# Kernel optimization log

Hardware: AMD Instinct MI355X
Metric: run time of the kernel (lower is better)

## Reference

```python
import jax, jax.numpy as jnp
import numpy as np

B, S, F_IN, F_OUT, K = 4, 4096, 64, 64, 32


def setup_inputs() -> dict:
    key = jax.random.key(0)
    k1, k2, k3 = jax.random.split(key, 3)
    X = jax.random.normal(k1, (B, S, F_IN), dtype=jnp.float32)
    M = jax.random.normal(k2, (B, S, K), dtype=jnp.float32)
    # xavier_uniform for weight: bound = sqrt(6/(fan_in+fan_out))
    bound = float(np.sqrt(6.0 / (F_IN + F_OUT)))
    weight = jax.random.uniform(k3, (F_IN, F_OUT), dtype=jnp.float32,
                                minval=-bound, maxval=bound)
    bias = jnp.zeros((F_OUT,), dtype=jnp.float32)
    return {"X": X, "M": M, "weight": weight, "bias": bias}


def reference(X, M, weight, bias):
    # similarity = softmax(relu(M M^T), axis=-1)  -> [B, S, S]
    sim_raw = jnp.einsum('bsk,btk->bst', M, M)
    sim = jax.nn.softmax(jax.nn.relu(sim_raw), axis=-1)
    # X W  -> [B, S, F_OUT]
    Xw = jnp.einsum('bsf,fo->bso', X, weight)
    # mode='add': (I + A) Xw = Xw + A @ Xw  (identity matmul folded)
    Z = Xw + jnp.einsum('bst,bto->bso', sim, Xw)
    Z = Z + bias
    # dropout is identity at inference (eval mode)
    return Z
```

## Files before the change

kernel.cpp:

```cpp
#include <hip/hip_runtime.h>
#include <cstdint>

#define BATCH  4
#define SLEN   4096
#define FDIM   64
#define KDIM   32
#define KSPLIT 8
#define CHUNK  (SLEN / KSPLIT)

typedef __attribute__((ext_vector_type(8))) short bf16x8;
typedef __attribute__((ext_vector_type(4))) float f32x4;

static __device__ __forceinline__ short f2bf(float f) {
    union { float f; unsigned u; } v; v.f = f;
    unsigned r = v.u + 0x7fffu + ((v.u >> 16) & 1u);
    return (short)(r >> 16);
}
static __device__ __forceinline__ float bf2f(short s) {
    union { unsigned u; float f; } v;
    v.u = ((unsigned)(unsigned short)s) << 16;
    return v.f;
}
static __device__ __forceinline__ unsigned pack2bf(float a, float b) {
    union { float f; unsigned u; } x, y; x.f = a; y.f = b;
    unsigned ra = x.u + 0x7fffu + ((x.u >> 16) & 1u);
    unsigned rb = y.u + 0x7fffu + ((y.u >> 16) & 1u);
    return __builtin_amdgcn_perm(rb, ra, 0x07060302u);
}

__global__ __launch_bounds__(256) void prep(const float4* __restrict__ M4,
                                            ushort4* __restrict__ H4,
                                            ushort4* __restrict__ L4,
                                            ushort4* __restrict__ QH4,
                                            ushort4* __restrict__ QL4,
                                            const float* __restrict__ X,
                                            const float4* __restrict__ W4,
                                            float4* __restrict__ V4,
                                            short* __restrict__ Vt) {
    const int blk = blockIdx.y * gridDim.x + blockIdx.x;
    const float LOG2E = 1.4426950408889634f;
#pragma unroll
    for (int r = 0; r < 2; ++r) {
        int i = (blk * 2 + r) * 256 + threadIdx.x;
        float4 m = M4[i];
        ushort4 h, l, sh, sl;
        h.x = (unsigned short)f2bf(m.x); l.x = (unsigned short)f2bf(m.x - bf2f((short)h.x));
        h.y = (unsigned short)f2bf(m.y); l.y = (unsigned short)f2bf(m.y - bf2f((short)h.y));
        h.z = (unsigned short)f2bf(m.z); l.z = (unsigned short)f2bf(m.z - bf2f((short)h.z));
        h.w = (unsigned short)f2bf(m.w); l.w = (unsigned short)f2bf(m.w - bf2f((short)h.w));
        float sx = m.x * LOG2E, sy = m.y * LOG2E, sz = m.z * LOG2E, sw = m.w * LOG2E;
        sh.x = (unsigned short)f2bf(sx); sl.x = (unsigned short)f2bf(sx - bf2f((short)sh.x));
        sh.y = (unsigned short)f2bf(sy); sl.y = (unsigned short)f2bf(sy - bf2f((short)sh.y));
        sh.z = (unsigned short)f2bf(sz); sl.z = (unsigned short)f2bf(sz - bf2f((short)sh.z));
        sh.w = (unsigned short)f2bf(sw); sl.w = (unsigned short)f2bf(sw - bf2f((short)sh.w));
        H4[i] = h; L4[i] = l; QH4[i] = sh; QL4[i] = sl;
    }
    __shared__ float t[64][65];
    const int b  = blockIdx.y;
    const int s0 = blockIdx.x * 64;
    const int o4 = threadIdx.x & 15;
    const int rq = threadIdx.x >> 4;
#pragma unroll
    for (int half = 0; half < 4; ++half) {
        int r = half * 16 + rq;
        const float* __restrict__ xr = X + ((size_t)b * SLEN + s0 + r) * FDIM;
        float4 acc = make_float4(0.f, 0.f, 0.f, 0.f);
#pragma unroll
        for (int f = 0; f < FDIM; ++f) {
            float4 w = W4[f * 16 + o4];
            float  x = xr[f];
            acc.x = fmaf(x, w.x, acc.x);
            acc.y = fmaf(x, w.y, acc.y);
            acc.z = fmaf(x, w.z, acc.z);
            acc.w = fmaf(x, w.w, acc.w);
        }
        V4[((size_t)b * SLEN + s0 + r) * 16 + o4] = acc;
        t[r][o4 * 4 + 0] = acc.x;
        t[r][o4 * 4 + 1] = acc.y;
        t[r][o4 * 4 + 2] = acc.z;
        t[r][o4 * 4 + 3] = acc.w;
    }
    __syncthreads();
    const int c0 = threadIdx.x & 63;
    const int r0 = threadIdx.x >> 6;
    const int pc = (c0 & 32) | (((c0 >> 2) & 3) << 3) | (((c0 >> 4) & 1) << 2)
                 | (c0 & 3);
#pragma unroll
    for (int i = 0; i < 16; ++i) {
        int f = r0 + i * 4;
        Vt[((size_t)b * FDIM + f) * SLEN + s0 + pc] = f2bf(t[c0][f]);
    }
}

__global__ __launch_bounds__(256, 4) void attn_mfma(const short* __restrict__ Mhi,
                                                    const short* __restrict__ Mlo,
                                                    const short* __restrict__ Qhi,
                                                    const short* __restrict__ Qlo,
                                                    const short* __restrict__ Vt,
                                                    float* __restrict__ accP,
                                                    float* __restrict__ lP) {
    const int bid  = blockIdx.x;
    const int slab = (bid & 7) + 8 * (bid >> 8);
    const int qblk = (bid >> 3) & 31;
    const int b    = slab >> 3;
    const int ks   = slab & 7;

    const int tid  = threadIdx.x;
    const int wave = tid >> 6;
    const int lane = tid & 63;
    const int col  = lane & 15;
    const int quad = lane >> 4;
    const int qbase = qblk * 128 + wave * 32;
    const int k0    = ks * CHUNK;

    const short* __restrict__ Mbh = Mhi + (size_t)b * SLEN * KDIM;
    const short* __restrict__ Mbl = Mlo + (size_t)b * SLEN * KDIM;
    const short* __restrict__ Qbh = Qhi + (size_t)b * SLEN * KDIM;
    const short* __restrict__ Qbl = Qlo + (size_t)b * SLEN * KDIM;
    const short* __restrict__ Vb  = Vt  + (size_t)b * FDIM * SLEN;

    __shared__ short khi[32 * 40];
    __shared__ short klo[32 * 40];
    __shared__ short vsh[64 * 40];

    bf16x8 Qh[2], Ql[2];
#pragma unroll
    for (int tq = 0; tq < 2; ++tq) {
        int qo = (qbase + tq * 16 + col) * KDIM + quad * 8;
        Qh[tq] = *(const bf16x8*)(Qbh + qo);
        Ql[tq] = *(const bf16x8*)(Qbl + qo);
    }

    const bf16x8 ONES = (bf16x8){0x3F80, 0x3F80, 0x3F80, 0x3F80,
                                 0x3F80, 0x3F80, 0x3F80, 0x3F80};

    f32x4 accf[2][4], accl[2];
#pragma unroll
    for (int tq = 0; tq < 2; ++tq) {
        accl[tq] = (f32x4){0.f, 0.f, 0.f, 0.f};
#pragma unroll
        for (int fg = 0; fg < 4; ++fg) accf[tq][fg] = (f32x4){0.f, 0.f, 0.f, 0.f};
    }

    const int krow  = (tid & 127) >> 2;
    const int kpart = tid & 3;
    const int vrow  = tid >> 2;
    const short* __restrict__ Msrc = (tid < 128) ? Mbh : Mbl;
    short* __restrict__ kdst = (tid < 128) ? khi : klo;

#pragma unroll 1
    for (int kt = k0; kt < k0 + CHUNK; kt += 32) {
        bf16x8 kstg = *(const bf16x8*)(Msrc + (kt + krow) * KDIM + kpart * 8);
        bf16x8 vstg = *(const bf16x8*)(Vb + (size_t)vrow * SLEN + kt + kpart * 8);
        __syncthreads();
        *(bf16x8*)(kdst + krow * 40 + kpart * 8) = kstg;
        *(bf16x8*)(vsh + vrow * 40 + kpart * 8)  = vstg;
        __syncthreads();

        bf16x8 Kh0 = *(const bf16x8*)(khi + col * 40 + quad * 8);
        bf16x8 Kh1 = *(const bf16x8*)(khi + (16 + col) * 40 + quad * 8);
        bf16x8 Kl0 = *(const bf16x8*)(klo + col * 40 + quad * 8);
        bf16x8 Kl1 = *(const bf16x8*)(klo + (16 + col) * 40 + quad * 8);
        bf16x8 Vv[4];
#pragma unroll
        for (int fg = 0; fg < 4; ++fg)
            Vv[fg] = *(const bf16x8*)(vsh + (fg * 16 + col) * 40 + quad * 8);

#pragma unroll
        for (int tq = 0; tq < 2; ++tq) {
            f32x4 z = (f32x4){0.f, 0.f, 0.f, 0.f};
            f32x4 c0 = __builtin_amdgcn_mfma_f32_16x16x32_bf16(Kh0, Ql[tq], z, 0, 0, 0);
            f32x4 c1 = __builtin_amdgcn_mfma_f32_16x16x32_bf16(Kh1, Ql[tq], z, 0, 0, 0);
            c0 = __builtin_amdgcn_mfma_f32_16x16x32_bf16(Kl0, Qh[tq], c0, 0, 0, 0);
            c1 = __builtin_amdgcn_mfma_f32_16x16x32_bf16(Kl1, Qh[tq], c1, 0, 0, 0);
            c0 = __builtin_amdgcn_mfma_f32_16x16x32_bf16(Kh0, Qh[tq], c0, 0, 0, 0);
            c1 = __builtin_amdgcn_mfma_f32_16x16x32_bf16(Kh1, Qh[tq], c1, 0, 0, 0);

            float e0 = __builtin_amdgcn_exp2f(fmaxf(c0[0], 0.f));
            float e1 = __builtin_amdgcn_exp2f(fmaxf(c0[1], 0.f));
            float e2 = __builtin_amdgcn_exp2f(fmaxf(c0[2], 0.f));
            float e3 = __builtin_amdgcn_exp2f(fmaxf(c0[3], 0.f));
            float e4 = __builtin_amdgcn_exp2f(fmaxf(c1[0], 0.f));
            float e5 = __builtin_amdgcn_exp2f(fmaxf(c1[1], 0.f));
            float e6 = __builtin_amdgcn_exp2f(fmaxf(c1[2], 0.f));
            float e7 = __builtin_amdgcn_exp2f(fmaxf(c1[3], 0.f));

            union { unsigned u[4]; bf16x8 v; } pa;
            pa.u[0] = pack2bf(e0, e1);
            pa.u[1] = pack2bf(e2, e3);
            pa.u[2] = pack2bf(e4, e5);
            pa.u[3] = pack2bf(e6, e7);

            accl[tq] = __builtin_amdgcn_mfma_f32_16x16x32_bf16(pa.v, ONES,
                                                               accl[tq], 0, 0, 0);
#pragma unroll
            for (int fg = 0; fg < 4; ++fg)
                accf[tq][fg] = __builtin_amdgcn_mfma_f32_16x16x32_bf16(
                    pa.v, Vv[fg], accf[tq][fg], 0, 0, 0);
        }
    }

#pragma unroll
    for (int tq = 0; tq < 2; ++tq) {
#pragma unroll
        for (int j = 0; j < 4; ++j) {
            int q = qbase + tq * 16 + quad * 4 + j;
            size_t base = ((size_t)b * SLEN + q) * KSPLIT + ks;
            float* __restrict__ op = accP + base * FDIM;
#pragma unroll
            for (int fg = 0; fg < 4; ++fg)
                op[fg * 16 + col] = accf[tq][fg][j];
            if (col == 0) lP[base] = accl[tq][j];
        }
    }
}

__global__ __launch_bounds__(256) void combine_kernel(const float4* __restrict__ V4,
                                                      const float4* __restrict__ accP4,
                                                      const float* __restrict__ lP,
                                                      const float4* __restrict__ bias4,
                                                      float4* __restrict__ out4) {
    int i  = blockIdx.x * 256 + threadIdx.x;
    int o4 = i & 15;
    int row = i >> 4;
    float nx = 0.f, ny = 0.f, nz = 0.f, nw = 0.f, den = 0.f;
#pragma unroll
    for (int k = 0; k < KSPLIT; ++k) {
        float4 a = accP4[((size_t)row * KSPLIT + k) * 16 + o4];
        nx += a.x; ny += a.y; nz += a.z; nw += a.w;
        den += lP[(size_t)row * KSPLIT + k];
    }
    float r = 1.f / den;
    float4 v = V4[i];
    float4 bb = bias4[o4];
    float4 o;
    o.x = v.x + nx * r + bb.x;
    o.y = v.y + ny * r + bb.y;
    o.z = v.z + nz * r + bb.z;
    o.w = v.w + nw * r + bb.w;
    out4[i] = o;
}

extern "C" void kernel_launch(void* const* d_in, const int* in_sizes, int n_in,
                              void* d_out, int out_size, void* d_ws, size_t ws_size,
                              hipStream_t stream) {
    const float* X    = (const float*)d_in[0];
    const float* M    = (const float*)d_in[1];
    const float* W    = (const float*)d_in[2];
    const float* bias = (const float*)d_in[3];
    float* out = (float*)d_out;

    const size_t vElems = (size_t)BATCH * SLEN * FDIM;
    const size_t mElems = (size_t)BATCH * SLEN * KDIM;
    const size_t rows   = (size_t)BATCH * SLEN;

    float* Vf   = (float*)d_ws;
    float* accP = Vf + vElems;
    float* lP   = accP + vElems * KSPLIT;
    short* Mhi  = (short*)(lP + rows * KSPLIT);
    short* Mlo  = Mhi + mElems;
    short* Qhi  = Mlo + mElems;
    short* Qlo  = Qhi + mElems;
    short* Vt   = Qlo + mElems;

    prep<<<dim3(SLEN / 64, BATCH), 256, 0, stream>>>(
        (const float4*)M, (ushort4*)Mhi, (ushort4*)Mlo,
        (ushort4*)Qhi, (ushort4*)Qlo,
        X, (const float4*)W, (float4*)Vf, Vt);

    attn_mfma<<<dim3((SLEN / 128) * BATCH * KSPLIT), 256, 0, stream>>>(
        Mhi, Mlo, Qhi, Qlo, Vt, accP, lP);

    combine_kernel<<<(int)(vElems / 1024), 256, 0, stream>>>(
        (const float4*)Vf, (const float4*)accP, lP, (const float4*)bias,
        (float4*)out);
}
```

Baseline: 122.5 us.

## Fuse split-K combine into attention kernel and load K/V directly from global

Folds the combine kernel into the attention kernel: each split-K block atomically bumps a per-query-block counter, and the last arriving block reduces the partial sums and writes the output. The LDS staging of K and V tiles and its barriers are removed, so each wave reads K and V fragments directly from global memory. The query tile per block doubles to 256 rows (64 per wave), halving the block count and lowering the occupancy hint to 2. This cuts a launch and the barriers but raises register pressure, adds redundant global loads per wave, and concentrates the reduction tail in a few blocks.

New measurement: 221.2 us. 80.5% more time.

```diff
diff --git a/kernel.cpp b/kernel.cpp
--- a/kernel.cpp
+++ b/kernel.cpp
@@ -7,6 +7,8 @@
 #define KDIM   32
 #define KSPLIT 8
 #define CHUNK  (SLEN / KSPLIT)
+#define QBLK   256
+#define NQB    (SLEN / QBLK)
 
 typedef __attribute__((ext_vector_type(8))) short bf16x8;
 typedef __attribute__((ext_vector_type(4))) float f32x4;
@@ -36,7 +38,11 @@
                                             const float* __restrict__ X,
                                             const float4* __restrict__ W4,
                                             float4* __restrict__ V4,
-                                            short* __restrict__ Vt) {
+                                            short* __restrict__ Vt,
+                                            int* __restrict__ cnt) {
+    if (blockIdx.y == 0 && threadIdx.x == 0)
+        cnt[blockIdx.x] = 0;
+
     const int blk = blockIdx.y * gridDim.x + blockIdx.x;
     const float LOG2E = 1.4426950408889634f;
 #pragma unroll
@@ -92,25 +98,31 @@
     }
 }
 
-__global__ __launch_bounds__(256, 4) void attn_mfma(const short* __restrict__ Mhi,
+__global__ __launch_bounds__(256, 2) void attn_mfma(const short* __restrict__ Mhi,
                                                     const short* __restrict__ Mlo,
                                                     const short* __restrict__ Qhi,
                                                     const short* __restrict__ Qlo,
                                                     const short* __restrict__ Vt,
                                                     float* __restrict__ accP,
-                                                    float* __restrict__ lP) {
+                                                    float* __restrict__ lP,
+                                                    const float4* __restrict__ V4,
+                                                    const float4* __restrict__ bias4,
+                                                    float4* __restrict__ out4,
+                                                    int* __restrict__ cnt) {
     const int bid  = blockIdx.x;
-    const int slab = (bid & 7) + 8 * (bid >> 8);
-    const int qblk = (bid >> 3) & 31;
-    const int b    = slab >> 3;
-    const int ks   = slab & 7;
+    const int xcd  = bid & 7;
+    const int slot = bid >> 3;
+    const int g    = xcd + 8 * (slot >> 4);
+    const int qblk = slot & 15;
+    const int b    = g >> 3;
+    const int ks   = g & 7;
 
     const int tid  = threadIdx.x;
     const int wave = tid >> 6;
     const int lane = tid & 63;
     const int col  = lane & 15;
     const int quad = lane >> 4;
-    const int qbase = qblk * 128 + wave * 32;
+    const int qbase = qblk * QBLK + wave * 64;
     const int k0    = ks * CHUNK;
 
     const short* __restrict__ Mbh = Mhi + (size_t)b * SLEN * KDIM;
@@ -119,13 +131,9 @@
     const short* __restrict__ Qbl = Qlo + (size_t)b * SLEN * KDIM;
     const short* __restrict__ Vb  = Vt  + (size_t)b * FDIM * SLEN;
 
-    __shared__ short khi[32 * 40];
-    __shared__ short klo[32 * 40];
-    __shared__ short vsh[64 * 40];
-
-    bf16x8 Qh[2], Ql[2];
-#pragma unroll
-    for (int tq = 0; tq < 2; ++tq) {
+    bf16x8 Qh[4], Ql[4];
+#pragma unroll
+    for (int tq = 0; tq < 4; ++tq) {
         int qo = (qbase + tq * 16 + col) * KDIM + quad * 8;
         Qh[tq] = *(const bf16x8*)(Qbh + qo);
         Ql[tq] = *(const bf16x8*)(Qbl + qo);
@@ -134,40 +142,27 @@
     const bf16x8 ONES = (bf16x8){0x3F80, 0x3F80, 0x3F80, 0x3F80,
                                  0x3F80, 0x3F80, 0x3F80, 0x3F80};
 
-    f32x4 accf[2][4], accl[2];
-#pragma unroll
-    for (int tq = 0; tq < 2; ++tq) {
+    f32x4 accf[4][4], accl[4];
+#pragma unroll
+    for (int tq = 0; tq < 4; ++tq) {
         accl[tq] = (f32x4){0.f, 0.f, 0.f, 0.f};
 #pragma unroll
         for (int fg = 0; fg < 4; ++fg) accf[tq][fg] = (f32x4){0.f, 0.f, 0.f, 0.f};
     }
-
-    const int krow  = (tid & 127) >> 2;
-    const int kpart = tid & 3;
-    const int vrow  = tid >> 2;
-    const short* __restrict__ Msrc = (tid < 128) ? Mbh : Mbl;
-    short* __restrict__ kdst = (tid < 128) ? khi : klo;
 
 #pragma unroll 1
     for (int kt = k0; kt < k0 + CHUNK; kt += 32) {
-        bf16x8 kstg = *(const bf16x8*)(Msrc + (kt + krow) * KDIM + kpart * 8);
-        bf16x8 vstg = *(const bf16x8*)(Vb + (size_t)vrow * SLEN + kt + kpart * 8);
-        __syncthreads();
-        *(bf16x8*)(kdst + krow * 40 + kpart * 8) = kstg;
-        *(bf16x8*)(vsh + vrow * 40 + kpart * 8)  = vstg;
-        __syncthreads();
-
-        bf16x8 Kh0 = *(const bf16x8*)(khi + col * 40 + quad * 8);
-        bf16x8 Kh1 = *(const bf16x8*)(khi + (16 + col) * 40 + quad * 8);
-        bf16x8 Kl0 = *(const bf16x8*)(klo + col * 40 + quad * 8);
-        bf16x8 Kl1 = *(const bf16x8*)(klo + (16 + col) * 40 + quad * 8);
+        const bf16x8 Kh0 = *(const bf16x8*)(Mbh + (kt + col) * KDIM + quad * 8);
+        const bf16x8 Kh1 = *(const bf16x8*)(Mbh + (kt + 16 + col) * KDIM + quad * 8);
+        const bf16x8 Kl0 = *(const bf16x8*)(Mbl + (kt + col) * KDIM + quad * 8);
+        const bf16x8 Kl1 = *(const bf16x8*)(Mbl + (kt + 16 + col) * KDIM + quad * 8);
         bf16x8 Vv[4];
 #pragma unroll
         for (int fg = 0; fg < 4; ++fg)
-            Vv[fg] = *(const bf16x8*)(vsh + (fg * 16 + col) * 40 + quad * 8);
-
-#pragma unroll
-        for (int tq = 0; tq < 2; ++tq) {
+            Vv[fg] = *(const bf16x8*)(Vb + (fg * 16 + col) * SLEN + kt + quad * 8);
+
+#pragma unroll
+        for (int tq = 0; tq < 4; ++tq) {
             f32x4 z = (f32x4){0.f, 0.f, 0.f, 0.f};
             f32x4 c0 = __builtin_amdgcn_mfma_f32_16x16x32_bf16(Kh0, Ql[tq], z, 0, 0, 0);
             f32x4 c1 = __builtin_amdgcn_mfma_f32_16x16x32_bf16(Kh1, Ql[tq], z, 0, 0, 0);
@@ -201,7 +196,7 @@
     }
 
 #pragma unroll
-    for (int tq = 0; tq < 2; ++tq) {
+    for (int tq = 0; tq < 4; ++tq) {
 #pragma unroll
         for (int j = 0; j < 4; ++j) {
             int q = qbase + tq * 16 + quad * 4 + j;
@@ -213,32 +208,41 @@
             if (col == 0) lP[base] = accl[tq][j];
         }
     }
-}
-
-__global__ __launch_bounds__(256) void combine_kernel(const float4* __restrict__ V4,
-                                                      const float4* __restrict__ accP4,
-                                                      const float* __restrict__ lP,
-                                                      const float4* __restrict__ bias4,
-                                                      float4* __restrict__ out4) {
-    int i  = blockIdx.x * 256 + threadIdx.x;
-    int o4 = i & 15;
-    int row = i >> 4;
-    float nx = 0.f, ny = 0.f, nz = 0.f, nw = 0.f, den = 0.f;
-#pragma unroll
-    for (int k = 0; k < KSPLIT; ++k) {
-        float4 a = accP4[((size_t)row * KSPLIT + k) * 16 + o4];
-        nx += a.x; ny += a.y; nz += a.z; nw += a.w;
-        den += lP[(size_t)row * KSPLIT + k];
-    }
-    float r = 1.f / den;
-    float4 v = V4[i];
-    float4 bb = bias4[o4];
-    float4 o;
-    o.x = v.x + nx * r + bb.x;
-    o.y = v.y + ny * r + bb.y;
-    o.z = v.z + nz * r + bb.z;
-    o.w = v.w + nw * r + bb.w;
-    out4[i] = o;
+
+    __threadfence();
+    __syncthreads();
+    __shared__ int lastFlag;
+    if (tid == 0) {
+        int old = atomicAdd(&cnt[b * NQB + qblk], 1);
+        lastFlag = (old == KSPLIT - 1) ? 1 : 0;
+    }
+    __syncthreads();
+    if (lastFlag) {
+        __threadfence();
+        const int o4   = tid & 15;
+        const int rsub = tid >> 4;
+        const float4 bb = bias4[o4];
+        const float4* __restrict__ accP4 = (const float4*)accP;
+#pragma unroll 1
+        for (int it = 0; it < 16; ++it) {
+            size_t row = (size_t)b * SLEN + qblk * QBLK + it * 16 + rsub;
+            float nx = 0.f, ny = 0.f, nz = 0.f, nw = 0.f, den = 0.f;
+#pragma unroll
+            for (int k = 0; k < KSPLIT; ++k) {
+                float4 a = accP4[(row * KSPLIT + k) * 16 + o4];
+                nx += a.x; ny += a.y; nz += a.z; nw += a.w;
+                den += lP[row * KSPLIT + k];
+            }
+            float rr = 1.f / den;
+            float4 v = V4[row * 16 + o4];
+            float4 o;
+            o.x = v.x + nx * rr + bb.x;
+            o.y = v.y + ny * rr + bb.y;
+            o.z = v.z + nz * rr + bb.z;
+            o.w = v.w + nw * rr + bb.w;
+            out4[row * 16 + o4] = o;
+        }
+    }
 }
 
 extern "C" void kernel_launch(void* const* d_in, const int* in_sizes, int n_in,
@@ -262,16 +266,14 @@
     short* Qhi  = Mlo + mElems;
     short* Qlo  = Qhi + mElems;
     short* Vt   = Qlo + mElems;
+    int*   cnt  = (int*)(Vt + vElems);
 
     prep<<<dim3(SLEN / 64, BATCH), 256, 0, stream>>>(
         (const float4*)M, (ushort4*)Mhi, (ushort4*)Mlo,
         (ushort4*)Qhi, (ushort4*)Qlo,
-        X, (const float4*)W, (float4*)Vf, Vt);
-
-    attn_mfma<<<dim3((SLEN / 128) * BATCH * KSPLIT), 256, 0, stream>>>(
-        Mhi, Mlo, Qhi, Qlo, Vt, accP, lP);
-
-    combine_kernel<<<(int)(vElems / 1024), 256, 0, stream>>>(
-        (const float4*)Vf, (const float4*)accP, lP, (const float4*)bias,
-        (float4*)out);
-}
+        X, (const float4*)W, (float4*)Vf, Vt, cnt);
+
+    attn_mfma<<<dim3(BATCH * KSPLIT * NQB), 256, 0, stream>>>(
+        Mhi, Mlo, Qhi, Qlo, Vt, accP, lP,
+        (const float4*)Vf, (const float4*)bias, (float4*)out, cnt);
+}
```
